# Optimization experiments

Measured on AMD Instinct MI355X. Metric: run time of the kernel, lower is better.

## Reference

```python
import jax, jax.numpy as jnp
import numpy as np

N_HEAD, D_MODEL, D_K, D_V = 16, 1024, 64, 64
B, S = 4, 2048
LN_EPS = 1e-5

def setup_inputs() -> dict:
    key = jax.random.key(0)
    ks = jax.random.split(key, 12)
    s = 1.0 / np.sqrt(D_MODEL)
    x = jax.random.normal(ks[0], (B, S, D_MODEL), dtype=jnp.float32)
    Wq = jax.random.normal(ks[1], (N_HEAD, D_MODEL, D_K), dtype=jnp.float32) * s
    bq = jax.random.normal(ks[2], (N_HEAD, D_K), dtype=jnp.float32) * 0.01
    Wk = jax.random.normal(ks[3], (N_HEAD, D_MODEL, D_K), dtype=jnp.float32) * s
    bk = jax.random.normal(ks[4], (N_HEAD, D_K), dtype=jnp.float32) * 0.01
    Wv = jax.random.normal(ks[5], (N_HEAD, D_MODEL, D_V), dtype=jnp.float32) * s
    bv = jax.random.normal(ks[6], (N_HEAD, D_V), dtype=jnp.float32) * 0.01
    Wfc = jax.random.normal(ks[7], (N_HEAD * D_V, D_MODEL), dtype=jnp.float32) * (1.0 / np.sqrt(N_HEAD * D_V))
    bfc = jax.random.normal(ks[8], (D_MODEL,), dtype=jnp.float32) * 0.01
    gamma = jnp.ones((D_MODEL,), dtype=jnp.float32)
    beta = jnp.zeros((D_MODEL,), dtype=jnp.float32)
    return {"x": x, "Wq": Wq, "bq": bq, "Wk": Wk, "bk": bk, "Wv": Wv, "bv": bv,
            "Wfc": Wfc, "bfc": bfc, "gamma": gamma, "beta": beta}

def reference(x, Wq, bq, Wk, bk, Wv, bv, Wfc, bfc, gamma, beta):
    # Per-head projections batched over heads: [B,H,S,d]
    q = jnp.einsum('bsd,hdk->bhsk', x, Wq) + bq[None, :, None, :]
    k = jnp.einsum('bsd,hdk->bhsk', x, Wk) + bk[None, :, None, :]
    v = jnp.einsum('bsd,hdv->bhsv', x, Wv) + bv[None, :, None, :]
    scores = jnp.einsum('bhqk,bhsk->bhqs', q, k) / jnp.sqrt(jnp.float32(D_K))
    probs = jax.nn.softmax(scores, axis=-1)
    attn = jnp.einsum('bhqs,bhsv->bhqv', probs, v)  # [B,H,S,Dv]
    # concat heads (cat along last dim == transpose heads to feature axis)
    cat = attn.transpose(0, 2, 1, 3).reshape(B, S, N_HEAD * D_V)
    y = cat @ Wfc + bfc
    mu = jnp.mean(y, axis=-1, keepdims=True)
    var = jnp.mean(jnp.square(y - mu), axis=-1, keepdims=True)
    return (y - mu) * jax.lax.rsqrt(var + LN_EPS) * gamma + beta
```

## Files before the change

### kernel.cpp

```cpp
#include <hip/hip_runtime.h>

#define NH 16
#define DMODEL 1024
#define DK 64
#define DV 64
#define BB 4
#define SS 2048
#define NTOK (BB*SS)
#define LN_EPS 1e-5f
#define SM_SHIFT 13.0f

typedef __attribute__((ext_vector_type(4))) float f32x4;
typedef __attribute__((ext_vector_type(8))) short s16x8;
typedef __attribute__((ext_vector_type(4))) short s16x4;

__device__ __forceinline__ short f2bf(float f) {
    union { float f; unsigned u; } a; a.f = f;
    unsigned r = a.u + 0x7FFFu + ((a.u >> 16) & 1u);
    return (short)(r >> 16);
}
__device__ __forceinline__ unsigned pk2(float a, float b) {
    union { float f; unsigned u; } x, y; x.f = a; y.f = b;
    return __builtin_amdgcn_perm(x.u + 0x8000u, y.u + 0x8000u, 0x07060302u);
}
__device__ __forceinline__ float fexp2(float x) { return __builtin_amdgcn_exp2f(x); }
__device__ __forceinline__ void gll16(const void* g, void* l) {
    __builtin_amdgcn_global_load_lds(
        (const __attribute__((address_space(1))) unsigned int*)g,
        (__attribute__((address_space(3))) unsigned int*)l, 16, 0, 0);
}

__global__ void k_cast_x(const float* __restrict__ x, short* __restrict__ xb) {
    int i = blockIdx.x * blockDim.x + threadIdx.x;
    f32x4 v = reinterpret_cast<const f32x4*>(x)[i];
    s16x4 o;
    o[0] = f2bf(v[0]); o[1] = f2bf(v[1]); o[2] = f2bf(v[2]); o[3] = f2bf(v[3]);
    reinterpret_cast<s16x4*>(xb)[i] = o;
}

__global__ __launch_bounds__(256) void k_conv_wqkv_t(const float* __restrict__ Wq,
                                                     const float* __restrict__ Wk,
                                                     const float* __restrict__ Wv,
                                                     short* __restrict__ WT) {
    __shared__ float tile[64][17];
    const int mh = blockIdx.y;
    const int mat = mh >> 4, h = mh & 15;
    const int dt = blockIdx.x >> 2, kt = blockIdx.x & 3;
    const float* src = (mat == 0 ? Wq : (mat == 1 ? Wk : Wv));
    const int t = threadIdx.x;
    #pragma unroll
    for (int p = 0; p < 4; p++) {
        int d = p * 16 + (t >> 4), kk = t & 15;
        tile[d][kk] = src[((size_t)h * 1024 + dt * 64 + d) * 64 + kt * 16 + kk];
    }
    __syncthreads();
    #pragma unroll
    for (int p = 0; p < 4; p++) {
        int kk = p * 4 + (t >> 6), d = t & 63;
        WT[((size_t)mat * 1024 + h * 64 + kt * 16 + kk) * 1024 + dt * 64 + d] = f2bf(tile[d][kk]);
    }
}

__global__ __launch_bounds__(256) void k_conv_wfc_t(const float* __restrict__ Wfc,
                                                    short* __restrict__ WfcT) {
    __shared__ float tile[64][17];
    const int ct = blockIdx.x >> 6, nt = blockIdx.x & 63;
    const int t = threadIdx.x;
    #pragma unroll
    for (int p = 0; p < 4; p++) {
        int c = p * 16 + (t >> 4), n = t & 15;
        tile[c][n] = Wfc[((size_t)ct * 64 + c) * 1024 + nt * 16 + n];
    }
    __syncthreads();
    #pragma unroll
    for (int p = 0; p < 4; p++) {
        int n = p * 4 + (t >> 6), c = t & 63;
        WfcT[((size_t)nt * 16 + n) * 1024 + ct * 64 + c] = f2bf(tile[c][n]);
    }
}

__global__ __launch_bounds__(512, 2) void k_gemm3(const short* __restrict__ A,
                                                  const short* __restrict__ BT,
                                                  const float* __restrict__ bq,
                                                  const float* __restrict__ bk,
                                                  short* __restrict__ Qb,
                                                  short* __restrict__ Kb) {
    __shared__ short lds[2][2][256][64];
    const int fid = blockIdx.x + blockIdx.y * 8;
    const int swz = (fid & 7) * 32 + (fid >> 3);
    const int gm0 = (swz >> 3) * 256, gn0 = (swz & 7) * 256;
    const int t = threadIdx.x, lane = t & 63, w = t >> 6;
    const int wm = w >> 2, wn = w & 3;
    const int lr = lane & 15, lg = lane >> 4;

    f32x4 acc[8][4] = {};

    const int lrow = t >> 3, gl = t & 7;
    const int sgx = (gl ^ (lrow & 7)) << 3;
    const short* pa = A  + (size_t)(gm0 + lrow) * 1024 + sgx;
    const short* pb = BT + (size_t)(gn0 + lrow) * 1024 + sgx;

    const int x7 = lr & 7;
    const int gx0 = (lg ^ x7) << 4;
    const int gx1 = ((4 + lg) ^ x7) << 4;

    char* a0 = (char*)lds[0][0]; char* b0 = (char*)lds[0][1];
    char* a1 = (char*)lds[1][0]; char* b1 = (char*)lds[1][1];

    auto STAGE = [&](int k0, char* dA, char* dB) {
        #pragma unroll
        for (int c = 0; c < 4; c++) {
            gll16(pa + (size_t)c * 65536 + k0, dA + c * 8192 + t * 16);
            gll16(pb + (size_t)c * 65536 + k0, dB + c * 8192 + t * 16);
        }
    };
    auto COMPUTE = [&](const char* bA, const char* bB) {
        s16x8 bF[4][2];
        #pragma unroll
        for (int n = 0; n < 4; n++) {
            const char* rp = bB + (wn * 64 + n * 16 + lr) * 128;
            bF[n][0] = *(const s16x8*)(rp + gx0);
            bF[n][1] = *(const s16x8*)(rp + gx1);
        }
        #pragma unroll
        for (int ph = 0; ph < 4; ph++) {
            s16x8 aF[2][2];
            #pragma unroll
            for (int mm = 0; mm < 2; mm++) {
                const char* rp = bA + (wm * 128 + (ph * 2 + mm) * 16 + lr) * 128;
                aF[mm][0] = *(const s16x8*)(rp + gx0);
                aF[mm][1] = *(const s16x8*)(rp + gx1);
            }
            __builtin_amdgcn_s_setprio(1);
            #pragma unroll
            for (int ks = 0; ks < 2; ks++)
                #pragma unroll
                for (int mm = 0; mm < 2; mm++)
                    #pragma unroll
                    for (int n = 0; n < 4; n++)
                        acc[ph * 2 + mm][n] = __builtin_amdgcn_mfma_f32_16x16x32_bf16(
                            aF[mm][ks], bF[n][ks], acc[ph * 2 + mm][n], 0, 0, 0);
            __builtin_amdgcn_s_setprio(0);
        }
    };

    STAGE(0, a0, b0);
    #pragma unroll 1
    for (int kt2 = 0; kt2 < 8; kt2++) {
        STAGE((2 * kt2 + 1) * 64, a1, b1);
        asm volatile("s_waitcnt vmcnt(8)" ::: "memory");
        __builtin_amdgcn_s_barrier();
        __builtin_amdgcn_sched_barrier(0);
        COMPUTE(a0, b0);
        __builtin_amdgcn_sched_barrier(0);
        __builtin_amdgcn_s_barrier();
        if (kt2 < 7) {
            STAGE((2 * kt2 + 2) * 64, a0, b0);
            asm volatile("s_waitcnt vmcnt(8)" ::: "memory");
        } else {
            asm volatile("s_waitcnt vmcnt(0)" ::: "memory");
        }
        __builtin_amdgcn_s_barrier();
        __builtin_amdgcn_sched_barrier(0);
        COMPUTE(a1, b1);
        __builtin_amdgcn_sched_barrier(0);
        __builtin_amdgcn_s_barrier();
    }

    short (*ct)[256] = (short(*)[256])lds;
    const float* bias = (gn0 < 1024) ? bq : bk;
    const int nloc0 = gn0 & 1023;
    const float scale = (gn0 < 1024) ? 0.18033688011112042f : 1.0f;
    float bval[4];
    #pragma unroll
    for (int n = 0; n < 4; n++) bval[n] = bias[nloc0 + wn * 64 + n * 16 + lr];

    #pragma unroll
    for (int m = 0; m < 8; m++)
        #pragma unroll
        for (int n = 0; n < 4; n++) {
            const int colg = wn * 4 + n;
            #pragma unroll
            for (int rg = 0; rg < 4; rg++) {
                int row = wm * 128 + m * 16 + lg * 4 + rg;
                int cg = colg ^ ((row << 1) & 15);
                ct[row][(cg << 4) + lr] = f2bf((acc[m][n][rg] + bval[n]) * scale);
            }
        }
    __syncthreads();

    short* dstM = (gn0 < 1024) ? Qb : Kb;
    const int qm = w >> 2, w4 = w & 3;
    #pragma unroll
    for (int qn = 0; qn < 2; qn++)
        #pragma unroll
        for (int rr = 0; rr < 2; rr++) {
            const int row = qm * 128 + w4 * 16 + (lane >> 2) + rr * 64;
            const int m = gm0 + row;
            const int b2 = m >> 11, s2 = m & 2047;
            #pragma unroll
            for (int j = 0; j < 4; j++) {
                const int cl = (lane & 3) + j * 4;
                const int chunk = qn * 16 + cl;
                const int cgs = (chunk >> 1) ^ ((row << 1) & 15);
                s16x8 v = *(const s16x8*)((char*)ct + row * 512 + (cgs << 5) + (chunk & 1) * 16);
                const int n0 = nloc0 + qn * 128 + cl * 8;
                const int h2 = n0 >> 6, kk = n0 & 63;
                *(s16x8*)(dstM + ((size_t)(b2 * NH + h2) * SS + s2) * DK + kk) = v;
            }
        }
}

template<int MODE, int NBX, int NWG, int GOFF>
__global__ __launch_bounds__(256) void k_gemm2(const short* __restrict__ A,
                                               const short* __restrict__ BT,
                                               const float* __restrict__ bq,
                                               const float* __restrict__ bk,
                                               const float* __restrict__ bv,
                                               const float* __restrict__ bfc,
                                               short* __restrict__ Qb,
                                               short* __restrict__ Kb,
                                               short* __restrict__ Vt,
                                               short* __restrict__ Yb) {
    __shared__ short smem[2][128][64];
    const int fid = blockIdx.x + blockIdx.y * NBX;
    const int swzid = (fid & 7) * (NWG / 8) + (fid >> 3);
    const int gm0 = (swzid / NBX) * 128, gn0 = (swzid % NBX) * 128 + GOFF;
    const int t = threadIdx.x, lane = t & 63, w = t >> 6;
    const int wm = w >> 1, wn = w & 1;
    const int lr = lane & 15, lg = lane >> 4;

    f32x4 acc[4][4] = {};

    const int lrow = t >> 3, gl = t & 7;
    const int sgx = (gl ^ (lrow & 7)) << 3;
    const short* pa = A  + (size_t)(gm0 + lrow) * 1024 + sgx;
    const short* pb = BT + (size_t)(gn0 + lrow) * 1024 + sgx;
    char* dA = (char*)smem[0] + w * 1024;
    char* dB = (char*)smem[1] + w * 1024;

    const int x7 = lr & 7;
    const int gx0 = (lg ^ x7) << 4;
    const int gx1 = ((4 + lg) ^ x7) << 4;

    for (int k0 = 0; k0 < 1024; k0 += 64) {
        #pragma unroll
        for (int c = 0; c < 4; c++) {
            gll16(pa + (size_t)c * 32768 + k0, dA + c * 4096);
            gll16(pb + (size_t)c * 32768 + k0, dB + c * 4096);
        }
        __syncthreads();
        s16x8 aF[2][4], bF[2][4];
        #pragma unroll
        for (int i = 0; i < 4; i++) {
            const char* rpa = (char*)smem[0] + (wm * 64 + i * 16 + lr) * 128;
            const char* rpb = (char*)smem[1] + (wn * 64 + i * 16 + lr) * 128;
            aF[0][i] = *(const s16x8*)(rpa + gx0);
            aF[1][i] = *(const s16x8*)(rpa + gx1);
            bF[0][i] = *(const s16x8*)(rpb + gx0);
            bF[1][i] = *(const s16x8*)(rpb + gx1);
        }
        __builtin_amdgcn_s_setprio(1);
        #pragma unroll
        for (int kk = 0; kk < 2; kk++)
            #pragma unroll
            for (int i = 0; i < 4; i++)
                #pragma unroll
                for (int j = 0; j < 4; j++)
                    acc[i][j] = __builtin_amdgcn_mfma_f32_16x16x32_bf16(aF[kk][i], bF[kk][j], acc[i][j], 0, 0, 0);
        __builtin_amdgcn_s_setprio(0);
        __syncthreads();
    }

    short (*ct)[128] = (short(*)[128])smem;
    const float* bias; int nloc0; float scale = 1.0f;
    if (MODE == 0) {
        if (gn0 < 1024)      { bias = bq; nloc0 = gn0;        scale = 0.18033688011112042f; }
        else if (gn0 < 2048) { bias = bk; nloc0 = gn0 - 1024; }
        else                 { bias = bv; nloc0 = gn0 - 2048; }
    } else { bias = bfc; nloc0 = gn0; }
    float bval[4];
    #pragma unroll
    for (int j = 0; j < 4; j++) bval[j] = bias[nloc0 + wn * 64 + j * 16 + lr];

    #pragma unroll
    for (int i = 0; i < 4; i++)
        #pragma unroll
        for (int j = 0; j < 4; j++) {
            const int colg = wn * 4 + j;
            #pragma unroll
            for (int rg = 0; rg < 4; rg++) {
                int row = wm * 64 + i * 16 + lg * 4 + rg;
                int cg = colg ^ ((row >> 1) & 7);
                ct[row][(cg << 4) + lr] = f2bf((acc[i][j][rg] + bval[j]) * scale);
            }
        }
    __syncthreads();

    if (MODE == 0 && GOFF >= 2048) {
        const int s0 = gm0 & 2047;
        const int b2v = gm0 >> 11;
        const int cg16 = lane >> 4;
        const int l16 = lane & 15;
        #pragma unroll
        for (int step = 0; step < 8; step++) {
            int c = w * 32 + step * 4 + cg16;
            int nl = (gn0 - 2048) + c;
            int h2 = nl >> 6, v = nl & 63;
            s16x8 o;
            #pragma unroll
            for (int j = 0; j < 8; j++) {
                int p = l16 * 8 + j;
                int blk = p >> 5, g = (p >> 3) & 3, h16 = (p >> 2) & 1, i2 = p & 3;
                int row = blk * 32 + h16 * 16 + g * 4 + i2;
                int cg2 = (c >> 4) ^ ((row >> 1) & 7);
                o[j] = ct[row][(cg2 << 4) + (c & 15)];
            }
            *(s16x8*)(Vt + ((size_t)(b2v * NH + h2) * 64 + v) * SS + s0 + l16 * 8) = o;
        }
    } else {
        short* dstM = (MODE == 0) ? (gn0 < 1024 ? Qb : Kb) : Yb;
        #pragma unroll
        for (int rr = 0; rr < 2; rr++) {
            const int row = w * 16 + (lane >> 2) + rr * 64;
            const int m = gm0 + row;
            const int swz = (row >> 1) & 7;
            #pragma unroll
            for (int j = 0; j < 4; j++) {
                const int c = (lane & 3) + j * 4;
                const int cg = (c >> 1) ^ swz;
                s16x8 v = *(const s16x8*)((char*)ct + row * 256 + (cg << 5) + (c & 1) * 16);
                if (MODE == 0) {
                    int b2 = m >> 11, s2 = m & 2047;
                    int n0 = (gn0 & 1023) + c * 8;
                    int h2 = n0 >> 6, kk = n0 & 63;
                    *(s16x8*)(dstM + ((size_t)(b2 * NH + h2) * SS + s2) * DK + kk) = v;
                } else {
                    *(s16x8*)(dstM + (size_t)m * 1024 + gn0 + c * 8) = v;
                }
            }
        }
    }
}

__global__ __launch_bounds__(512) void k_attn2(const short* __restrict__ Qb,
                                               const short* __restrict__ Kb,
                                               const short* __restrict__ VT2,
                                               short* __restrict__ cat) {
    __shared__ char smem[2][16384];
    const int fid = blockIdx.x + blockIdx.y * gridDim.x;
    const int swz = ((fid & 7) << 6) | (fid >> 3);
    const int qt = swz & 7, bh = swz >> 3;
    const int b = bh >> 4, h = bh & 15;
    const int t = threadIdx.x, lane = t & 63, w = t >> 6;
    const int lr = lane & 15, lg = lane >> 4;

    const short* Qbase = Qb + ((size_t)bh * SS + qt * 256 + w * 32) * DK;
    s16x8 qF[2][2];
    #pragma unroll
    for (int f = 0; f < 2; f++) {
        qF[f][0] = *(const s16x8*)(Qbase + (f * 16 + lr) * DK + lg * 8);
        qF[f][1] = *(const s16x8*)(Qbase + (f * 16 + lr) * DK + 32 + lg * 8);
    }
    s16x8 onesF;
    #pragma unroll
    for (int i = 0; i < 8; i++) onesF[i] = (short)0x3F80;

    const char* Kbase = (const char*)(Kb + (size_t)bh * SS * DK);
    const char* Vbase = (const char*)(VT2 + (size_t)bh * DK * SS);
    const int rk = w * 8 + (lane >> 3);
    const int gl = lane & 7;
    const char* pK = Kbase + rk * 128 + ((gl ^ (rk & 7)) << 4);
    const char* pV = Vbase + rk * (SS * 2) + ((gl ^ (rk & 7)) << 4);

    const int x7 = lr & 7;
    const int gx0 = (lg ^ x7) << 4;
    const int gx1 = ((4 + lg) ^ x7) << 4;

    f32x4 acc[2][4] = {};
    f32x4 accs[2] = {};
    const f32x4 zinit = {-SM_SHIFT, -SM_SHIFT, -SM_SHIFT, -SM_SHIFT};

    {
        char* d = smem[0];
        gll16(pK, d + w * 1024);
        gll16(pV, d + 8192 + w * 1024);
    }
    __syncthreads();

    int cur = 0;
    for (int kt = 0; kt < SS; kt += 64) {
        if (kt + 64 < SS) {
            char* d = smem[cur ^ 1];
            gll16(pK + (kt + 64) * 128, d + w * 1024);
            gll16(pV + (kt + 64) * 2,   d + 8192 + w * 1024);
        }
        const char* bs = smem[cur];

        s16x8 kA[4][2];
        #pragma unroll
        for (int kg = 0; kg < 4; kg++) {
            const char* rp = bs + (kg * 16 + lr) * 128;
            kA[kg][0] = *(const s16x8*)(rp + gx0);
            kA[kg][1] = *(const s16x8*)(rp + gx1);
        }
        f32x4 st[2][4];
        __builtin_amdgcn_s_setprio(1);
        #pragma unroll
        for (int f = 0; f < 2; f++)
            #pragma unroll
            for (int kg = 0; kg < 4; kg++) {
                f32x4 z = __builtin_amdgcn_mfma_f32_16x16x32_bf16(kA[kg][0], qF[f][0], zinit, 0, 0, 0);
                st[f][kg] = __builtin_amdgcn_mfma_f32_16x16x32_bf16(kA[kg][1], qF[f][1], z, 0, 0, 0);
            }
        __builtin_amdgcn_s_setprio(0);

        s16x8 pb[2][2];
        #pragma unroll
        for (int f = 0; f < 2; f++) {
            float p[4][4];
            #pragma unroll
            for (int kg = 0; kg < 4; kg++)
                #pragma unroll
                for (int rg = 0; rg < 4; rg++)
                    p[kg][rg] = fexp2(st[f][kg][rg]);
            #pragma unroll
            for (int ks = 0; ks < 2; ks++) {
                union { s16x8 v; unsigned u[4]; } U;
                U.u[0] = pk2(p[2 * ks][1],     p[2 * ks][0]);
                U.u[1] = pk2(p[2 * ks][3],     p[2 * ks][2]);
                U.u[2] = pk2(p[2 * ks + 1][1], p[2 * ks + 1][0]);
                U.u[3] = pk2(p[2 * ks + 1][3], p[2 * ks + 1][2]);
                pb[f][ks] = U.v;
            }
        }

        __builtin_amdgcn_s_setprio(1);
        #pragma unroll
        for (int f = 0; f < 2; f++) {
            accs[f] = __builtin_amdgcn_mfma_f32_16x16x32_bf16(onesF, pb[f][0], accs[f], 0, 0, 0);
            accs[f] = __builtin_amdgcn_mfma_f32_16x16x32_bf16(onesF, pb[f][1], accs[f], 0, 0, 0);
        }
        #pragma unroll
        for (int vt = 0; vt < 4; vt++) {
            const char* rp = bs + 8192 + (vt * 16 + lr) * 128;
            s16x8 vA0 = *(const s16x8*)(rp + gx0);
            s16x8 vA1 = *(const s16x8*)(rp + gx1);
            #pragma unroll
            for (int f = 0; f < 2; f++) {
                acc[f][vt] = __builtin_amdgcn_mfma_f32_16x16x32_bf16(vA0, pb[f][0], acc[f][vt], 0, 0, 0);
                acc[f][vt] = __builtin_amdgcn_mfma_f32_16x16x32_bf16(vA1, pb[f][1], acc[f][vt], 0, 0, 0);
            }
        }
        __builtin_amdgcn_s_setprio(0);
        __syncthreads();
        cur ^= 1;
    }

    char* ods = (char*)smem + w * 4096;
    float inv[2] = {1.0f / accs[0][0], 1.0f / accs[1][0]};
    #pragma unroll
    for (int f = 0; f < 2; f++)
        #pragma unroll
        for (int vt = 0; vt < 4; vt++)
            #pragma unroll
            for (int rg = 0; rg < 4; rg++)
                *(short*)(ods + (f * 16 + lr) * 128 + (vt * 16 + lg * 4 + rg) * 2) =
                    f2bf(acc[f][vt][rg] * inv[f]);
    __syncthreads();
    {
        int r = lane >> 1, hb = lane & 1;
        const char* srow = (char*)smem + w * 4096 + r * 128 + hb * 64;
        int token = b * SS + qt * 256 + w * 32 + r;
        char* dst = (char*)(cat + (size_t)token * 1024 + h * 64 + hb * 32);
        #pragma unroll
        for (int i = 0; i < 4; i++)
            *(s16x8*)(dst + i * 16) = *(const s16x8*)(srow + i * 16);
    }
}

__global__ __launch_bounds__(256) void k_ln(const short* __restrict__ Yb,
                                            const float* __restrict__ gamma,
                                            const float* __restrict__ beta,
                                            float* __restrict__ out) {
    const int row = blockIdx.x;
    const int t = threadIdx.x;
    s16x4 raw = reinterpret_cast<const s16x4*>(Yb + (size_t)row * 1024)[t];
    float v[4];
    #pragma unroll
    for (int i = 0; i < 4; i++) {
        union { unsigned u; float f; } cvt;
        cvt.u = ((unsigned)(unsigned short)raw[i]) << 16;
        v[i] = cvt.f;
    }
    float s = v[0] + v[1] + v[2] + v[3];
    float s2 = v[0] * v[0] + v[1] * v[1] + v[2] * v[2] + v[3] * v[3];
    #pragma unroll
    for (int off = 32; off; off >>= 1) {
        s += __shfl_xor(s, off);
        s2 += __shfl_xor(s2, off);
    }
    __shared__ float red[8];
    int w = t >> 6, lane = t & 63;
    if (lane == 0) { red[w] = s; red[4 + w] = s2; }
    __syncthreads();
    float S = red[0] + red[1] + red[2] + red[3];
    float S2 = red[4] + red[5] + red[6] + red[7];
    float mu = S * (1.f / 1024.f);
    float var = S2 * (1.f / 1024.f) - mu * mu;
    float rs = rsqrtf(var + LN_EPS);
    f32x4 g = reinterpret_cast<const f32x4*>(gamma)[t];
    f32x4 be = reinterpret_cast<const f32x4*>(beta)[t];
    f32x4 o;
    #pragma unroll
    for (int i = 0; i < 4; i++) o[i] = (v[i] - mu) * rs * g[i] + be[i];
    reinterpret_cast<f32x4*>(out + (size_t)row * 1024)[t] = o;
}

extern "C" void kernel_launch(void* const* d_in, const int* in_sizes, int n_in,
                              void* d_out, int out_size, void* d_ws, size_t ws_size,
                              hipStream_t stream) {
    const float* x    = (const float*)d_in[0];
    const float* Wq   = (const float*)d_in[1];
    const float* bq   = (const float*)d_in[2];
    const float* Wk   = (const float*)d_in[3];
    const float* bk   = (const float*)d_in[4];
    const float* Wv   = (const float*)d_in[5];
    const float* bv   = (const float*)d_in[6];
    const float* Wfc  = (const float*)d_in[7];
    const float* bfc  = (const float*)d_in[8];
    const float* gamma= (const float*)d_in[9];
    const float* beta = (const float*)d_in[10];
    float* out = (float*)d_out;

    char* p = (char*)d_ws;
    short* xb   = (short*)p; p += (size_t)NTOK * 1024 * 2;
    short* WT   = (short*)p; p += (size_t)3072 * 1024 * 2;
    short* WfcT = (short*)p; p += (size_t)1024 * 1024 * 2;
    short* Qb   = (short*)p; p += (size_t)64 * SS * 64 * 2;
    short* Kb   = (short*)p; p += (size_t)64 * SS * 64 * 2;
    short* Vb   = (short*)p; p += (size_t)64 * SS * 64 * 2;
    short* VTb  = (short*)p; p += (size_t)64 * 64 * SS * 2;
    short* cat  = (short*)p; p += (size_t)NTOK * 1024 * 2;
    short* Yb   = Qb;
    (void)Vb;

    k_cast_x     <<<NTOK * 1024 / 4 / 256, 256, 0, stream>>>(x, xb);
    k_conv_wqkv_t<<<dim3(64, 48), 256, 0, stream>>>(Wq, Wk, Wv, WT);
    k_conv_wfc_t <<<1024, 256, 0, stream>>>(Wfc, WfcT);
    k_gemm3      <<<dim3(8, 32), 512, 0, stream>>>(xb, WT, bq, bk, Qb, Kb);
    k_gemm2<0, 8, 512, 2048><<<dim3(8, 64), 256, 0, stream>>>(xb, WT, bq, bk, bv, nullptr, Qb, Kb, VTb, nullptr);
    k_attn2      <<<dim3(8, 64), 512, 0, stream>>>(Qb, Kb, VTb, cat);
    k_gemm2<1, 8, 512, 0><<<dim3(8, 64), 256, 0, stream>>>(cat, WfcT, nullptr, nullptr, nullptr, bfc, nullptr, nullptr, nullptr, Yb);
    k_ln         <<<NTOK, 256, 0, stream>>>(Yb, gamma, beta, out);
}
```

Baseline: 179.4 us.

## Replace output-projection GEMM with 128x256-tile double-buffered 512-thread kernel

The output projection (cat @ Wfc + bias) moves from the generic 128x128 k_gemm2 kernel to a new k_gemm4 that uses 128x256 tiles with 8 waves. It stages A and B tiles into swizzled LDS through direct global-to-LDS loads, double-buffered with explicit vmcnt waits so loads overlap MFMA work. The larger tile raises operand reuse per LDS load and halves the number of workgroups, but uses more LDS and registers per block, which may limit occupancy.

```diff
diff --git a/kernel.cpp b/kernel.cpp
--- a/kernel.cpp
+++ b/kernel.cpp
@@ -209,6 +209,119 @@
                 *(s16x8*)(dstM + ((size_t)(b2 * NH + h2) * SS + s2) * DK + kk) = v;
             }
         }
+}
+
+__global__ __launch_bounds__(512, 2) void k_gemm4(const short* __restrict__ A,
+                                                  const short* __restrict__ BT,
+                                                  const float* __restrict__ bfc,
+                                                  short* __restrict__ Yb) {
+    __shared__ short lds[2][24576];
+    const int fid = blockIdx.x + blockIdx.y * 8;
+    const int swz = (fid & 7) * 32 + (fid >> 3);
+    const int gm0 = (swz >> 2) * 128, gn0 = (swz & 3) * 256;
+    const int t = threadIdx.x, lane = t & 63, w = t >> 6;
+    const int wm = w >> 2, wn = w & 3;
+    const int lr = lane & 15, lg = lane >> 4;
+
+    f32x4 acc[4][4] = {};
+
+    const int lrow = t >> 3, gl = t & 7;
+    const int sgx = (gl ^ (lrow & 7)) << 3;
+    const short* pa = A  + (size_t)(gm0 + lrow) * 1024 + sgx;
+    const short* pb = BT + (size_t)(gn0 + lrow) * 1024 + sgx;
+
+    const int x7 = lr & 7;
+    const int gx0 = (lg ^ x7) << 4;
+    const int gx1 = ((4 + lg) ^ x7) << 4;
+
+    char* a0 = (char*)lds[0];          char* b0 = (char*)lds[0] + 16384;
+    char* a1 = (char*)lds[1];          char* b1 = (char*)lds[1] + 16384;
+
+    auto STAGE = [&](int k0, char* dA, char* dB) {
+        #pragma unroll
+        for (int c = 0; c < 2; c++)
+            gll16(pa + (size_t)c * 65536 + k0, dA + c * 8192 + t * 16);
+        #pragma unroll
+        for (int c = 0; c < 4; c++)
+            gll16(pb + (size_t)c * 65536 + k0, dB + c * 8192 + t * 16);
+    };
+    auto COMPUTE = [&](const char* bA, const char* bB) {
+        s16x8 bF[4][2];
+        #pragma unroll
+        for (int n = 0; n < 4; n++) {
+            const char* rp = bB + (wn * 64 + n * 16 + lr) * 128;
+            bF[n][0] = *(const s16x8*)(rp + gx0);
+            bF[n][1] = *(const s16x8*)(rp + gx1);
+        }
+        #pragma unroll
+        for (int m = 0; m < 4; m++) {
+            s16x8 aF[2];
+            const char* rp = bA + (wm * 64 + m * 16 + lr) * 128;
+            aF[0] = *(const s16x8*)(rp + gx0);
+            aF[1] = *(const s16x8*)(rp + gx1);
+            __builtin_amdgcn_s_setprio(1);
+            #pragma unroll
+            for (int ks = 0; ks < 2; ks++)
+                #pragma unroll
+                for (int n = 0; n < 4; n++)
+                    acc[m][n] = __builtin_amdgcn_mfma_f32_16x16x32_bf16(
+                        aF[ks], bF[n][ks], acc[m][n], 0, 0, 0);
+            __builtin_amdgcn_s_setprio(0);
+        }
+    };
+
+    STAGE(0, a0, b0);
+    #pragma unroll 1
+    for (int kt2 = 0; kt2 < 8; kt2++) {
+        STAGE((2 * kt2 + 1) * 64, a1, b1);
+        asm volatile("s_waitcnt vmcnt(6)" ::: "memory");
+        __builtin_amdgcn_s_barrier();
+        __builtin_amdgcn_sched_barrier(0);
+        COMPUTE(a0, b0);
+        __builtin_amdgcn_sched_barrier(0);
+        __builtin_amdgcn_s_barrier();
+        if (kt2 < 7) {
+            STAGE((2 * kt2 + 2) * 64, a0, b0);
+            asm volatile("s_waitcnt vmcnt(6)" ::: "memory");
+        } else {
+            asm volatile("s_waitcnt vmcnt(0)" ::: "memory");
+        }
+        __builtin_amdgcn_s_barrier();
+        __builtin_amdgcn_sched_barrier(0);
+        COMPUTE(a1, b1);
+        __builtin_amdgcn_sched_barrier(0);
+        __builtin_amdgcn_s_barrier();
+    }
+
+    short (*ct)[256] = (short(*)[256])lds;
+    float bval[4];
+    #pragma unroll
+    for (int n = 0; n < 4; n++) bval[n] = bfc[gn0 + wn * 64 + n * 16 + lr];
+    #pragma unroll
+    for (int m = 0; m < 4; m++)
+        #pragma unroll
+        for (int n = 0; n < 4; n++) {
+            const int colg = wn * 4 + n;
+            #pragma unroll
+            for (int rg = 0; rg < 4; rg++) {
+                int row = wm * 64 + m * 16 + lg * 4 + rg;
+                int cg = colg ^ ((row << 1) & 15);
+                ct[row][(cg << 4) + lr] = f2bf(acc[m][n][rg] + bval[n]);
+            }
+        }
+    __syncthreads();
+
+    {
+        const int row = w * 16 + (lane >> 2);
+        const int m = gm0 + row;
+        #pragma unroll
+        for (int j = 0; j < 8; j++) {
+            const int chunk = (lane & 3) + j * 4;
+            const int cgs = (chunk >> 1) ^ ((row << 1) & 15);
+            s16x8 v = *(const s16x8*)((char*)ct + row * 512 + (cgs << 5) + (chunk & 1) * 16);
+            *(s16x8*)(Yb + (size_t)m * 1024 + gn0 + chunk * 8) = v;
+        }
+    }
 }
 
 template<int MODE, int NBX, int NWG, int GOFF>
@@ -551,6 +664,6 @@
     k_gemm3      <<<dim3(8, 32), 512, 0, stream>>>(xb, WT, bq, bk, Qb, Kb);
     k_gemm2<0, 8, 512, 2048><<<dim3(8, 64), 256, 0, stream>>>(xb, WT, bq, bk, bv, nullptr, Qb, Kb, VTb, nullptr);
     k_attn2      <<<dim3(8, 64), 512, 0, stream>>>(Qb, Kb, VTb, cat);
-    k_gemm2<1, 8, 512, 0><<<dim3(8, 64), 256, 0, stream>>>(cat, WfcT, nullptr, nullptr, nullptr, bfc, nullptr, nullptr, nullptr, Yb);
+    k_gemm4      <<<dim3(8, 32), 512, 0, stream>>>(cat, WfcT, bfc, Yb);
     k_ln         <<<NTOK, 256, 0, stream>>>(Yb, gamma, beta, out);
 }
```

Measured after the change: 179.8 us (median of 2 runs). About the same (+0.2%).
